# Kernel tuning notes

Measured on AMD Instinct MI355X. Metric: run time of the kernel, lower is better.

Reference implementation:

```python
import jax, jax.numpy as jnp
import numpy as np

SR = 16000
NUM_MEL = 80
FRAME_LEN = 400
FRAME_SHIFT = 160
PADDED_WIN = 512         # next pow2 of 400
NUM_FFT_BINS = PADDED_WIN // 2 + 1  # 257
PREEMPH = 0.97
EPS = 1e-6


def _mel_scale(f):
    return 1127.0 * np.log(1.0 + f / 700.0)


def _get_mel_banks(num_bins, window_padded, sample_freq, low_freq=20.0, high_freq=0.0):
    # Faithful port of torchaudio.compliance.kaldi.get_mel_banks (vtln_warp=1.0)
    num_fft_bins = window_padded // 2  # 256 (last bin padded with zero later)
    nyquist = 0.5 * sample_freq
    if high_freq <= 0.0:
        high_freq = nyquist + high_freq
    fft_bin_width = sample_freq / window_padded
    mel_low = _mel_scale(low_freq)
    mel_high = _mel_scale(high_freq)
    mel_delta = (mel_high - mel_low) / (num_bins + 1)
    left = mel_low + np.arange(num_bins, dtype=np.float64)[:, None] * mel_delta
    center = left + mel_delta
    right = center + mel_delta
    mel = _mel_scale(fft_bin_width * np.arange(num_fft_bins, dtype=np.float64))[None, :]
    up = (mel - left) / (center - left)
    down = (right - mel) / (right - center)
    bins = np.maximum(0.0, np.minimum(up, down))
    return bins.astype(np.float32)  # [num_bins, window_padded//2]


def _make_buffers():
    n = np.arange(FRAME_LEN, dtype=np.float32)
    window = (0.54 - 0.46 * np.cos(2 * np.pi * n / (FRAME_LEN - 1))).astype(np.float32)
    t = np.arange(PADDED_WIN, dtype=np.float32)
    f = np.arange(NUM_FFT_BINS, dtype=np.float32)[:, None]
    angles = 2.0 * np.pi * f * t / PADDED_WIN
    dft_real = np.cos(angles).astype(np.float32)        # [257, 512]
    dft_imag = (-np.sin(angles)).astype(np.float32)     # [257, 512]
    mel = _get_mel_banks(NUM_MEL, PADDED_WIN, float(SR))
    mel_weight = np.pad(mel, ((0, 0), (0, 1)))          # [80, 257]
    return window, dft_real, dft_imag, mel_weight


def setup_inputs() -> dict:
    key = jax.random.key(0)
    waveform = jax.random.normal(key, (32, 480000), dtype=jnp.float32)
    window, dft_real, dft_imag, mel_weight = _make_buffers()
    return {
        "waveform": waveform,
        "window": jnp.asarray(window),
        "dft_real": jnp.asarray(dft_real),
        "dft_imag": jnp.asarray(dft_imag),
        "mel_weight": jnp.asarray(mel_weight),
    }


def reference(waveform, window, dft_real, dft_imag, mel_weight):
    B, T = waveform.shape
    num_frames = (T - FRAME_LEN) // FRAME_SHIFT + 1
    # Framing (equivalent to conv1d with identity kernel, stride=FRAME_SHIFT)
    idx = jnp.arange(num_frames)[:, None] * FRAME_SHIFT + jnp.arange(FRAME_LEN)
    frames = waveform[:, idx].reshape(B * num_frames, FRAME_LEN)  # [BF, 400]
    # dither == 0 -> skipped
    # remove DC offset
    frames = frames - jnp.mean(frames, axis=1, keepdims=True)
    # raw energy (computed by the original module; unused since use_energy=False)
    _log_energy = jnp.log(jnp.maximum(jnp.sum(frames * frames, axis=1), EPS))
    # preemphasis with replicate left pad
    prev = jnp.concatenate([frames[:, :1], frames[:, :-1]], axis=1)
    frames = frames - PREEMPH * prev
    # Hamming window + zero pad to 512
    frames = frames * window[None, :]
    frames = jnp.pad(frames, ((0, 0), (0, PADDED_WIN - FRAME_LEN)))  # [BF, 512]
    # Brute-force DFT as matmuls
    real = frames @ dft_real.T  # [BF, 257]
    imag = frames @ dft_imag.T  # [BF, 257]
    power = real * real + imag * imag
    # Mel projection + log
    mel = power @ mel_weight.T + EPS  # [BF, 80]
    mel = jnp.log(jnp.maximum(mel, EPS))
    return mel.reshape(B, num_frames, NUM_MEL)
```

## Files before the change

kernel.cpp:

```cpp
#include <hip/hip_runtime.h>
#include <math.h>


#define BATCH 32
#define TLEN 480000
#define NFRAMES 2998
#define FL 400
#define FS 160
#define PW 512
#define NM 80
#define MT 32
#define NTILES 94
#define PRE 0.97f
#define EPSF 1e-6f

#define RE_KS 9
#define IM_KS 8
#define RE_U16 (16 * RE_KS * 64 * 8)
#define IM_U16 (16 * IM_KS * 64 * 8)
#define MEL_U16 (6 * 8 * 64 * 8)
#define OFF_REH 0
#define OFF_REL RE_U16
#define OFF_IMH (2 * RE_U16)
#define OFF_IML (2 * RE_U16 + IM_U16)
#define OFF_MEL (2 * RE_U16 + 2 * IM_U16)
#define OFF_CS  (OFF_MEL + MEL_U16)
#define WS_NEED ((size_t)OFF_CS * 2 + 512 * 4)

#define C0_SH 0
#define C0_SL 8704
#define C0_DH 17408
#define C0_DL 26112
#define C1_SH 0
#define C1_SL 10240
#define C1_DH 20480
#define C1_DL 29184

typedef short bf16x8 __attribute__((ext_vector_type(8)));
typedef float f32x4 __attribute__((ext_vector_type(4)));
typedef unsigned int u32;
typedef unsigned short u16;
typedef u32 u32x4 __attribute__((ext_vector_type(4)));

__device__ __forceinline__ u16 f2bf(float f) {
    u32 u = __builtin_bit_cast(u32, f);
    return (u16)((u + 0x7FFFu + ((u >> 16) & 1u)) >> 16);
}
__device__ __forceinline__ float bf2f(u16 h) {
    u32 u = ((u32)h) << 16;
    return __builtin_bit_cast(float, u);
}

__global__ void prep_kernel(const float* __restrict__ dftr, const float* __restrict__ dfti,
                            const float* __restrict__ melw, u16* __restrict__ wsb) {
    int idx = blockIdx.x * 256 + threadIdx.x;
    if (idx < 16 * RE_KS * 64) {
        int nf = idx / (RE_KS * 64);
        int rem = idx - nf * (RE_KS * 64);
        int ks = rem >> 6, l = rem & 63;
        int f = nf * 16 + (l & 15);
        int k = ks * 32 + ((l >> 4) << 3);
        u16* dh = wsb + OFF_REH + (size_t)idx * 8;
        u16* dl = wsb + OFF_REL + (size_t)idx * 8;
        #pragma unroll
        for (int e = 0; e < 8; ++e) {
            int kk = k + e;
            float x = (kk <= 256) ? dftr[(size_t)f * PW + kk] : 0.f;
            u16 h = f2bf(x);
            dh[e] = h;
            dl[e] = f2bf(x - bf2f(h));
        }
    } else if (idx < 16 * RE_KS * 64 + 16 * IM_KS * 64) {
        int j = idx - 16 * RE_KS * 64;
        int nf = j / (IM_KS * 64);
        int rem = j - nf * (IM_KS * 64);
        int ks = rem >> 6, l = rem & 63;
        int f = nf * 16 + (l & 15);
        int k = ks * 32 + ((l >> 4) << 3);
        u16* dh = wsb + OFF_IMH + (size_t)j * 8;
        u16* dl = wsb + OFF_IML + (size_t)j * 8;
        #pragma unroll
        for (int e = 0; e < 8; ++e) {
            float x = dfti[(size_t)f * PW + k + e];
            u16 h = f2bf(x);
            dh[e] = h;
            dl[e] = f2bf(x - bf2f(h));
        }
    } else {
        int m = idx - (16 * RE_KS * 64 + 16 * IM_KS * 64);
        if (m < 6 * 8 * 64) {
            int nf = m / (8 * 64);
            int ks = (m >> 6) & 7, l = m & 63;
            int n = nf * 16 + (l & 15);
            int k = ks * 32 + ((l >> 4) << 3);
            u16* dst = wsb + OFF_MEL + (size_t)m * 8;
            #pragma unroll
            for (int e = 0; e < 8; ++e)
                dst[e] = (n < NM) ? f2bf(melw[(size_t)n * 257 + k + e]) : (u16)0;
        }
    }
}

__global__ void prep_cs_kernel(const float* __restrict__ dftr, const float* __restrict__ dfti,
                               const float* __restrict__ win, u16* __restrict__ wsb) {
    const int gw = (blockIdx.x * 256 + threadIdx.x) >> 6;
    const int lane = threadIdx.x & 63;
    float* cs = (float*)(wsb + OFF_CS);
    float acc = 0.f;
    if (gw < 256) {
        const int f = gw;
        for (int t = lane; t <= 256; t += 64) {
            float wt = (t < FL) ? win[t] : 0.f;
            float wu = (t >= 1 && t < 256 && (512 - t) < FL) ? win[512 - t] : 0.f;
            acc += (wt + wu) * dftr[(size_t)f * PW + t];
        }
    } else {
        const int ff = gw - 256;
        for (int t = lane; t <= 255; t += 64) {
            float wt = (t < FL) ? win[t] : 0.f;
            float wu = (t >= 1 && (512 - t) < FL) ? win[512 - t] : 0.f;
            acc += (wt - wu) * dfti[(size_t)ff * PW + t];
        }
    }
    #pragma unroll
    for (int o = 32; o; o >>= 1) acc += __shfl_xor(acc, o);
    if (lane == 0) cs[gw] = acc;
}

__device__ __forceinline__ u32 swz(int SWT, u32 r) {
    return (SWT == 0) ? ((r & 7u) << 4) : (SWT == 1) ? (((r >> 1) & 3u) << 4) : 0u;
}

#define MFMA6(D, J)                                                                        \
    _Pragma("unroll")                                                                      \
    for (int mf = 0; mf < 2; ++mf) {                                                       \
        acc[mf][J] = __builtin_amdgcn_mfma_f32_16x16x32_bf16(aH[mf], D[0], acc[mf][J], 0, 0, 0); \
        acc[mf][J] = __builtin_amdgcn_mfma_f32_16x16x32_bf16(aL[mf], D[0], acc[mf][J], 0, 0, 0); \
        acc[mf][J] = __builtin_amdgcn_mfma_f32_16x16x32_bf16(aH[mf], D[1], acc[mf][J], 0, 0, 0); \
    }

template<int RS, int SWT, int NKS, int BKS>
__device__ __forceinline__ void dft_pass(
    const char* tH, const char* tL,
    const u16* __restrict__ bH, const u16* __restrict__ bL,
    int ks0, int w, int lane, f32x4 (&acc)[2][2]) {

    bf16x8 aH[2], aL[2], Ba[2], Bb[2];

#define LDA_P(KS)                                                              \
    { _Pragma("unroll")                                                        \
      for (int mf = 0; mf < 2; ++mf) {                                         \
        u32 r = (u32)(mf * 16 + (lane & 15));                                  \
        u32 off = (u32)((KS) * 64 + ((lane >> 4) << 4));                       \
        u32 byte = r * RS + (off ^ swz(SWT, r));                               \
        aH[mf] = *(const bf16x8*)(tH + byte);                                  \
        aL[mf] = *(const bf16x8*)(tL + byte);                                  \
      } }
#define LDB_P(KSG, J, D)                                                       \
    {                                                                          \
        size_t o = ((size_t)((2 * w + (J)) * BKS + (KSG)) * 64 + lane) * 8;    \
        D[0] = *(const bf16x8*)(bH + o);                                       \
        D[1] = *(const bf16x8*)(bL + o);                                       \
    }

    LDB_P(ks0, 0, Ba);
    #pragma unroll
    for (int ks = 0; ks < NKS; ++ks) {
        LDA_P(ks);
        LDB_P(ks0 + ks, 1, Bb);
        MFMA6(Ba, 0);
        if (ks + 1 < NKS) LDB_P(ks0 + ks + 1, 0, Ba);
        MFMA6(Bb, 1);
    }
#undef LDA_P
#undef LDB_P
}

__device__ __forceinline__ void pack_write(const float* ys, char* baseH, char* baseL, u32 byte) {
    u32x4 hv, lv;
    #pragma unroll
    for (int e = 0; e < 4; ++e) {
        u16 h0 = f2bf(ys[2 * e]), h1 = f2bf(ys[2 * e + 1]);
        hv[e] = (u32)h0 | ((u32)h1 << 16);
        u16 l0 = f2bf(ys[2 * e] - bf2f(h0)), l1 = f2bf(ys[2 * e + 1] - bf2f(h1));
        lv[e] = (u32)l0 | ((u32)l1 << 16);
    }
    *(u32x4*)(baseH + byte) = hv;
    *(u32x4*)(baseL + byte) = lv;
}

__global__ __launch_bounds__(512, 4) void fbank_mfma(
    const float* __restrict__ wave, const float* __restrict__ win,
    const u16* __restrict__ wsb, float* __restrict__ out) {
    __shared__ float smean[MT];
    __shared__ u16 stile[18944];
    char* T = (char*)stile;

    const int tid = threadIdx.x, w = tid >> 6, lane = tid & 63;
    const int q = lane >> 4;
    const int cg = lane & 15;
    const int b = blockIdx.y;
    const int f0 = blockIdx.x * MT;
    const float* wb = wave + (size_t)b * TLEN;
    const float4* win4 = (const float4*)win;

    const int rr = w * 4 + q;
    const int fr = f0 + rr;
    const bool valid = fr < NFRAMES;
    const float* x = wb + (size_t)fr * FS;
    const float4* x4 = (const float4*)x;
    float ps = 0.f;

    {
        float4 v0 = {0,0,0,0}, v1 = {0,0,0,0};
        if (valid) { v0 = x4[2 * cg]; v1 = x4[2 * cg + 1]; }
        ps += v0.x + v0.y + v0.z + v0.w + v1.x + v1.y + v1.z + v1.w;
        float4 w0 = win4[2 * cg], w1 = win4[2 * cg + 1];
        float xpn = __shfl(v1.w, lane - 1);
        float xprev = (cg == 0) ? v0.x : xpn;
        float y[8];
        y[0] = (v0.x - PRE * xprev) * w0.x;
        y[1] = (v0.y - PRE * v0.x) * w0.y;
        y[2] = (v0.z - PRE * v0.y) * w0.z;
        y[3] = (v0.w - PRE * v0.z) * w0.w;
        y[4] = (v1.x - PRE * v0.w) * w1.x;
        y[5] = (v1.y - PRE * v1.x) * w1.y;
        y[6] = (v1.z - PRE * v1.y) * w1.z;
        y[7] = (v1.w - PRE * v1.z) * w1.w;

        float yr[8];
        #pragma unroll
        for (int e = 0; e < 8; ++e) yr[e] = 0.f;
        if (cg >= 14) {
            const int u0 = 512 - 8 * cg;
            float4 xr0 = {0,0,0,0}, xr1 = {0,0,0,0};
            float xu0 = 0.f;
            if (valid) {
                xr0 = x4[u0 / 4 - 2]; xr1 = x4[u0 / 4 - 1];
                if (u0 <= 399) xu0 = x[u0];
            }
            ps += xr0.x + xr0.y + xr0.z + xr0.w + xr1.x + xr1.y + xr1.z + xr1.w;
            float4 wr0 = win4[u0 / 4 - 2], wr1 = win4[u0 / 4 - 1];
            float wu0 = (u0 <= 399) ? win[u0] : 0.f;
            yr[0] = (xu0   - PRE * xr1.w) * wu0;
            yr[1] = (xr1.w - PRE * xr1.z) * wr1.w;
            yr[2] = (xr1.z - PRE * xr1.y) * wr1.z;
            yr[3] = (xr1.y - PRE * xr1.x) * wr1.y;
            yr[4] = (xr1.x - PRE * xr0.w) * wr1.x;
            yr[5] = (xr0.w - PRE * xr0.z) * wr0.w;
            yr[6] = (xr0.z - PRE * xr0.y) * wr0.z;
            yr[7] = (xr0.y - PRE * xr0.x) * wr0.y;
        }
        float s8[8], d8[8];
        #pragma unroll
        for (int e = 0; e < 8; ++e) { s8[e] = y[e] + yr[e]; d8[e] = y[e] - yr[e]; }
        u32 byte = (u32)rr * 272u + (u32)cg * 16u;
        pack_write(s8, T + C0_SH, T + C0_SL, byte);
        pack_write(d8, T + C0_DH, T + C0_DL, byte);
    }
    __syncthreads();

    f32x4 accR[2][2], accI[2][2];
    #pragma unroll
    for (int mf = 0; mf < 2; ++mf)
        #pragma unroll
        for (int j = 0; j < 2; ++j) { accR[mf][j] = (f32x4)0.f; accI[mf][j] = (f32x4)0.f; }

    dft_pass<272, 2, 4, RE_KS>(T + C0_SH, T + C0_SL, wsb + OFF_REH, wsb + OFF_REL, 0, w, lane, accR);
    dft_pass<272, 2, 4, IM_KS>(T + C0_DH, T + C0_DL, wsb + OFF_IMH, wsb + OFF_IML, 0, w, lane, accI);
    __syncthreads();

    {
        float4 v0 = {0,0,0,0}, v1 = {0,0,0,0};
        if (valid) { v0 = x4[32 + 2 * cg]; v1 = x4[33 + 2 * cg]; }
        ps += v0.x + v0.y + v0.z + v0.w + v1.x + v1.y + v1.z + v1.w;
        float4 w0 = win4[32 + 2 * cg], w1 = win4[33 + 2 * cg];
        float xpn = __shfl(v1.w, lane - 1);
        float xprev = (cg == 0) ? (valid ? x[127] : 0.f) : xpn;
        float y[8];
        y[0] = (v0.x - PRE * xprev) * w0.x;
        y[1] = (v0.y - PRE * v0.x) * w0.y;
        y[2] = (v0.z - PRE * v0.y) * w0.z;
        y[3] = (v0.w - PRE * v0.z) * w0.w;
        y[4] = (v1.x - PRE * v0.w) * w1.x;
        y[5] = (v1.y - PRE * v1.x) * w1.y;
        y[6] = (v1.z - PRE * v1.y) * w1.z;
        y[7] = (v1.w - PRE * v1.z) * w1.w;

        const int u0 = 384 - 8 * cg;
        float4 xr0 = {0,0,0,0}, xr1 = {0,0,0,0};
        float xu0 = 0.f;
        if (valid) { xr0 = x4[u0 / 4 - 2]; xr1 = x4[u0 / 4 - 1]; xu0 = x[u0]; }
        ps += xr0.x + xr0.y + xr0.z + xr0.w + xr1.x + xr1.y + xr1.z + xr1.w;
        float4 wr0 = win4[u0 / 4 - 2], wr1 = win4[u0 / 4 - 1];
        float wu0 = win[u0];
        float yr[8];
        yr[0] = (xu0   - PRE * xr1.w) * wu0;
        yr[1] = (xr1.w - PRE * xr1.z) * wr1.w;
        yr[2] = (xr1.z - PRE * xr1.y) * wr1.z;
        yr[3] = (xr1.y - PRE * xr1.x) * wr1.y;
        yr[4] = (xr1.x - PRE * xr0.w) * wr1.x;
        yr[5] = (xr0.w - PRE * xr0.z) * wr0.w;
        yr[6] = (xr0.z - PRE * xr0.y) * wr0.z;
        yr[7] = (xr0.y - PRE * xr0.x) * wr0.y;

        float s8[8], d8[8];
        #pragma unroll
        for (int e = 0; e < 8; ++e) { s8[e] = y[e] + yr[e]; d8[e] = y[e] - yr[e]; }
        u32 byteS = (u32)rr * 320u + (((u32)cg * 16u) ^ ((((u32)rr >> 1) & 3u) << 4));
        u32 byteD = (u32)rr * 272u + (u32)cg * 16u;
        pack_write(s8, T + C1_SH, T + C1_SL, byteS);
        pack_write(d8, T + C1_DH, T + C1_DL, byteD);

        float acc = ps;
        #pragma unroll
        for (int o = 8; o; o >>= 1) acc += __shfl_xor(acc, o);
        if (cg == 0) smean[rr] = acc * (1.0f / FL);
    }
    {
        const int trr = tid & 31;
        const int grp = tid >> 5;
        if (grp < 4) {
            const int tfr = f0 + trr;
            float y256 = 0.f;
            if (grp == 0 && tfr < NFRAMES) {
                const float* tx = wb + (size_t)tfr * FS;
                y256 = (tx[256] - PRE * tx[255]) * win[256];
            }
            float s8[8] = {y256, 0.f, 0.f, 0.f, 0.f, 0.f, 0.f, 0.f};
            u32 byte = (u32)trr * 320u + ((((u32)(16 + grp)) * 16u) ^ ((((u32)trr >> 1) & 3u) << 4));
            pack_write(s8, T + C1_SH, T + C1_SL, byte);
        }
    }
    __syncthreads();

    dft_pass<320, 1, 5, RE_KS>(T + C1_SH, T + C1_SL, wsb + OFF_REH, wsb + OFF_REL, 4, w, lane, accR);
    dft_pass<272, 2, 4, IM_KS>(T + C1_DH, T + C1_DL, wsb + OFF_IMH, wsb + OFF_IML, 4, w, lane, accI);
    __syncthreads();

    {
        const float* cs = (const float*)(wsb + OFF_CS);
        #pragma unroll
        for (int mf = 0; mf < 2; ++mf)
            #pragma unroll
            for (int j = 0; j < 2; ++j) {
                const u32 bin = (u32)(32 * w + j * 16 + cg);
                const float Cb = cs[bin], Sb = cs[256 + bin];
                #pragma unroll
                for (int r = 0; r < 4; ++r) {
                    u32 row = (u32)(mf * 16 + (q << 2) + r);
                    const float mcr = (1.0f - PRE) * smean[row];
                    float pR = accR[mf][j][r] - mcr * Cb;
                    float pI = accI[mf][j][r] - mcr * Sb;
                    float pw = pR * pR + pI * pI;
                    u32 byte = (row * 512u + bin * 2u) ^ ((row & 7u) << 4);
                    *(u16*)(T + byte) = f2bf(pw);
                }
            }
    }
    __syncthreads();

    const u16* melb = wsb + OFF_MEL;
    if (w < 6) {
        const int mfm = w & 1;
        const int nf0 = (w >> 1) * 2;
        f32x4 accM[2];
        #pragma unroll
        for (int j = 0; j < 2; ++j) accM[j] = (f32x4)0.f;
        for (int ks = 0; ks < 8; ++ks) {
            u32 row = (u32)(mfm * 16 + cg);
            u32 byte = (row * 512u + (u32)(ks * 32 + (q << 3)) * 2u) ^ ((row & 7u) << 4);
            bf16x8 aP = *(const bf16x8*)(T + byte);
            #pragma unroll
            for (int j = 0; j < 2; ++j) {
                bf16x8 bM = *(const bf16x8*)(melb + ((size_t)((nf0 + j) * 8 + ks) * 64 + lane) * 8);
                accM[j] = __builtin_amdgcn_mfma_f32_16x16x32_bf16(aP, bM, accM[j], 0, 0, 0);
            }
        }
        #pragma unroll
        for (int j = 0; j < 2; ++j) {
            const int m = (nf0 + j) * 16 + cg;
            #pragma unroll
            for (int r = 0; r < 4; ++r) {
                const int rowl = mfm * 16 + (q << 2) + r;
                const int ofr = f0 + rowl;
                if (ofr < NFRAMES && m < NM) {
                    float v = fmaxf(accM[j][r] + EPSF, EPSF);
                    out[((size_t)b * NFRAMES + ofr) * NM + m] = logf(v);
                }
            }
        }
    }
}

#define TFB 16
#define NB 256
__global__ __launch_bounds__(256, 3) void fbank_fallback(
    const float* __restrict__ wave, const float* __restrict__ win,
    const float* __restrict__ dftr, const float* __restrict__ dfti,
    const float* __restrict__ melw, float* __restrict__ out) {
    __shared__ float s_fr[TFB][PW];
    __shared__ float s_pw[TFB][NB + 1];
    const int tid = threadIdx.x, wv = tid >> 6, lane = tid & 63;
    const int fbase = blockIdx.x * TFB;
    #pragma unroll
    for (int j = 0; j < TFB / 4; ++j) {
        const int lf = wv * (TFB / 4) + j;
        const int gid = fbase + lf;
        const int bb = gid / NFRAMES;
        const int fr = gid - bb * NFRAMES;
        const float* x = wave + (size_t)bb * TLEN + (size_t)fr * FS;
        float s = 0.f;
        for (int i = lane; i < FL; i += 64) s += x[i];
        #pragma unroll
        for (int off = 32; off >= 1; off >>= 1) s += __shfl_xor(s, off);
        const float mean = s * (1.0f / FL);
        for (int i = lane; i < FL; i += 64) {
            const float xi = x[i];
            const float xm = (i == 0) ? xi : x[i - 1];
            s_fr[lf][i] = (xi - PRE * xm - (1.0f - PRE) * mean) * win[i];
        }
        for (int i = FL + lane; i < PW; i += 64) s_fr[lf][i] = 0.f;
    }
    __syncthreads();
    {
        const int bin = tid;
        const float4* dr4 = (const float4*)(dftr + (size_t)bin * PW);
        const float4* di4 = (const float4*)(dfti + (size_t)bin * PW);
        float accr[TFB], acci[TFB];
        #pragma unroll
        for (int f = 0; f < TFB; ++f) { accr[f] = 0.f; acci[f] = 0.f; }
        for (int k4 = 0; k4 < PW / 4; ++k4) {
            const float4 r = dr4[k4], im = di4[k4];
            #pragma unroll
            for (int f = 0; f < TFB; ++f) {
                const float4 fr = *(const float4*)&s_fr[f][k4 * 4];
                accr[f] += fr.x * r.x + fr.y * r.y + fr.z * r.z + fr.w * r.w;
                acci[f] += fr.x * im.x + fr.y * im.y + fr.z * im.z + fr.w * im.w;
            }
        }
        #pragma unroll
        for (int f = 0; f < TFB; ++f) s_pw[f][bin] = accr[f] * accr[f] + acci[f] * acci[f];
    }
    __syncthreads();
    for (int o = tid; o < TFB * NM; o += 256) {
        const int f = o / NM, m = o - f * NM;
        const float* wm = melw + (size_t)m * 257;
        float acc = 0.f;
        for (int k = 0; k < NB; ++k) acc += s_pw[f][k] * wm[k];
        out[(size_t)(fbase + f) * NM + m] = logf(fmaxf(acc + EPSF, EPSF));
    }
}

extern "C" void kernel_launch(void* const* d_in, const int* in_sizes, int n_in,
                              void* d_out, int out_size, void* d_ws, size_t ws_size,
                              hipStream_t stream) {
    const float* wave = (const float*)d_in[0];
    const float* win  = (const float*)d_in[1];
    const float* dftr = (const float*)d_in[2];
    const float* dfti = (const float*)d_in[3];
    const float* melw = (const float*)d_in[4];
    float* out = (float*)d_out;

    if (ws_size >= WS_NEED) {
        u16* wsb = (u16*)d_ws;
        const int prep_threads = 16 * RE_KS * 64 + 16 * IM_KS * 64 + 6 * 8 * 64;
        prep_kernel<<<(prep_threads + 255) / 256, 256, 0, stream>>>(dftr, dfti, melw, wsb);
        prep_cs_kernel<<<128, 256, 0, stream>>>(dftr, dfti, win, wsb);
        dim3 grid(NTILES, BATCH);
        fbank_mfma<<<grid, 512, 0, stream>>>(wave, win, wsb, out);
    } else {
        const int nblocks = (BATCH * NFRAMES) / TFB;
        fbank_fallback<<<nblocks, 256, 0, stream>>>(wave, win, dftr, dfti, melw, out);
    }
}
```

Baseline: 119.1 us.

## Enlarge frame tile to 48 rows and use hardware bf16 pack conversion

Raises the per-block frame tile from 32 to 48 rows, so each wave runs three M-fragments per DFT pass. Each bf16 B-fragment loaded from global memory is then reused across more MFMAs, and there are fewer blocks overall. The packing and mel stages are restructured so the first four waves handle the extra 16 rows. The software float-to-bf16 rounding is replaced by the v_cvt_pk_bf16_f32 instruction. In exchange, LDS use and register pressure grow, which may lower occupancy under the 512x4 launch bounds, and waves 4-7 sit idle during the extra packing.

```diff
diff --git a/kernel.cpp b/kernel.cpp
--- a/kernel.cpp
+++ b/kernel.cpp
@@ -9,8 +9,8 @@
 #define FS 160
 #define PW 512
 #define NM 80
-#define MT 32
-#define NTILES 94
+#define MT 48
+#define NTILES 63
 #define PRE 0.97f
 #define EPSF 1e-6f
 
@@ -28,13 +28,13 @@
 #define WS_NEED ((size_t)OFF_CS * 2 + 512 * 4)
 
 #define C0_SH 0
-#define C0_SL 8704
-#define C0_DH 17408
-#define C0_DL 26112
+#define C0_SL 13056
+#define C0_DH 26112
+#define C0_DL 39168
 #define C1_SH 0
-#define C1_SL 10240
-#define C1_DH 20480
-#define C1_DL 29184
+#define C1_SL 15360
+#define C1_DH 30720
+#define C1_DL 43776
 
 typedef short bf16x8 __attribute__((ext_vector_type(8)));
 typedef float f32x4 __attribute__((ext_vector_type(4)));
@@ -49,6 +49,11 @@
 __device__ __forceinline__ float bf2f(u16 h) {
     u32 u = ((u32)h) << 16;
     return __builtin_bit_cast(float, u);
+}
+__device__ __forceinline__ u32 cvtpk2(float lo, float hi) {
+    u32 r;
+    asm("v_cvt_pk_bf16_f32 %0, %1, %2" : "=v"(r) : "v"(lo), "v"(hi));
+    return r;
 }
 
 __global__ void prep_kernel(const float* __restrict__ dftr, const float* __restrict__ dfti,
@@ -131,25 +136,25 @@
     return (SWT == 0) ? ((r & 7u) << 4) : (SWT == 1) ? (((r >> 1) & 3u) << 4) : 0u;
 }
 
-#define MFMA6(D, J)                                                                        \
+#define MFMA9(D, J)                                                                        \
     _Pragma("unroll")                                                                      \
-    for (int mf = 0; mf < 2; ++mf) {                                                       \
+    for (int mf = 0; mf < 3; ++mf) {                                                       \
         acc[mf][J] = __builtin_amdgcn_mfma_f32_16x16x32_bf16(aH[mf], D[0], acc[mf][J], 0, 0, 0); \
         acc[mf][J] = __builtin_amdgcn_mfma_f32_16x16x32_bf16(aL[mf], D[0], acc[mf][J], 0, 0, 0); \
         acc[mf][J] = __builtin_amdgcn_mfma_f32_16x16x32_bf16(aH[mf], D[1], acc[mf][J], 0, 0, 0); \
     }
 
 template<int RS, int SWT, int NKS, int BKS>
-__device__ __forceinline__ void dft_pass(
+__device__ __forceinline__ void dft_pass3(
     const char* tH, const char* tL,
     const u16* __restrict__ bH, const u16* __restrict__ bL,
-    int ks0, int w, int lane, f32x4 (&acc)[2][2]) {
-
-    bf16x8 aH[2], aL[2], Ba[2], Bb[2];
+    int ks0, int w, int lane, f32x4 (&acc)[3][2]) {
+
+    bf16x8 aH[3], aL[3], Ba[2], Bb[2];
 
 #define LDA_P(KS)                                                              \
     { _Pragma("unroll")                                                        \
-      for (int mf = 0; mf < 2; ++mf) {                                         \
+      for (int mf = 0; mf < 3; ++mf) {                                         \
         u32 r = (u32)(mf * 16 + (lane & 15));                                  \
         u32 off = (u32)((KS) * 64 + ((lane >> 4) << 4));                       \
         u32 byte = r * RS + (off ^ swz(SWT, r));                               \
@@ -168,9 +173,9 @@
     for (int ks = 0; ks < NKS; ++ks) {
         LDA_P(ks);
         LDB_P(ks0 + ks, 1, Bb);
-        MFMA6(Ba, 0);
+        MFMA9(Ba, 0);
         if (ks + 1 < NKS) LDB_P(ks0 + ks + 1, 0, Ba);
-        MFMA6(Bb, 1);
+        MFMA9(Bb, 1);
     }
 #undef LDA_P
 #undef LDB_P
@@ -180,121 +185,56 @@
     u32x4 hv, lv;
     #pragma unroll
     for (int e = 0; e < 4; ++e) {
-        u16 h0 = f2bf(ys[2 * e]), h1 = f2bf(ys[2 * e + 1]);
-        hv[e] = (u32)h0 | ((u32)h1 << 16);
-        u16 l0 = f2bf(ys[2 * e] - bf2f(h0)), l1 = f2bf(ys[2 * e + 1] - bf2f(h1));
-        lv[e] = (u32)l0 | ((u32)l1 << 16);
+        float y0 = ys[2 * e], y1 = ys[2 * e + 1];
+        u32 h = cvtpk2(y0, y1);
+        hv[e] = h;
+        float h0 = __builtin_bit_cast(float, h << 16);
+        float h1 = __builtin_bit_cast(float, h & 0xFFFF0000u);
+        lv[e] = cvtpk2(y0 - h0, y1 - h1);
     }
     *(u32x4*)(baseH + byte) = hv;
     *(u32x4*)(baseL + byte) = lv;
 }
 
-__global__ __launch_bounds__(512, 4) void fbank_mfma(
-    const float* __restrict__ wave, const float* __restrict__ win,
-    const u16* __restrict__ wsb, float* __restrict__ out) {
-    __shared__ float smean[MT];
-    __shared__ u16 stile[18944];
-    char* T = (char*)stile;
-
-    const int tid = threadIdx.x, w = tid >> 6, lane = tid & 63;
-    const int q = lane >> 4;
-    const int cg = lane & 15;
-    const int b = blockIdx.y;
-    const int f0 = blockIdx.x * MT;
-    const float* wb = wave + (size_t)b * TLEN;
-    const float4* win4 = (const float4*)win;
-
-    const int rr = w * 4 + q;
+__device__ __forceinline__ float pack_c0(const float* wb, const float4* win4,
+                                         const float* win, char* T,
+                                         int f0, int rr, int lane, int cg) {
     const int fr = f0 + rr;
     const bool valid = fr < NFRAMES;
     const float* x = wb + (size_t)fr * FS;
     const float4* x4 = (const float4*)x;
     float ps = 0.f;
 
-    {
-        float4 v0 = {0,0,0,0}, v1 = {0,0,0,0};
-        if (valid) { v0 = x4[2 * cg]; v1 = x4[2 * cg + 1]; }
-        ps += v0.x + v0.y + v0.z + v0.w + v1.x + v1.y + v1.z + v1.w;
-        float4 w0 = win4[2 * cg], w1 = win4[2 * cg + 1];
-        float xpn = __shfl(v1.w, lane - 1);
-        float xprev = (cg == 0) ? v0.x : xpn;
-        float y[8];
-        y[0] = (v0.x - PRE * xprev) * w0.x;
-        y[1] = (v0.y - PRE * v0.x) * w0.y;
-        y[2] = (v0.z - PRE * v0.y) * w0.z;
-        y[3] = (v0.w - PRE * v0.z) * w0.w;
-        y[4] = (v1.x - PRE * v0.w) * w1.x;
-        y[5] = (v1.y - PRE * v1.x) * w1.y;
-        y[6] = (v1.z - PRE * v1.y) * w1.z;
-        y[7] = (v1.w - PRE * v1.z) * w1.w;
-
-        float yr[8];
-        #pragma unroll
-        for (int e = 0; e < 8; ++e) yr[e] = 0.f;
-        if (cg >= 14) {
-            const int u0 = 512 - 8 * cg;
-            float4 xr0 = {0,0,0,0}, xr1 = {0,0,0,0};
-            float xu0 = 0.f;
-            if (valid) {
-                xr0 = x4[u0 / 4 - 2]; xr1 = x4[u0 / 4 - 1];
-                if (u0 <= 399) xu0 = x[u0];
-            }
-            ps += xr0.x + xr0.y + xr0.z + xr0.w + xr1.x + xr1.y + xr1.z + xr1.w;
-            float4 wr0 = win4[u0 / 4 - 2], wr1 = win4[u0 / 4 - 1];
-            float wu0 = (u0 <= 399) ? win[u0] : 0.f;
-            yr[0] = (xu0   - PRE * xr1.w) * wu0;
-            yr[1] = (xr1.w - PRE * xr1.z) * wr1.w;
-            yr[2] = (xr1.z - PRE * xr1.y) * wr1.z;
-            yr[3] = (xr1.y - PRE * xr1.x) * wr1.y;
-            yr[4] = (xr1.x - PRE * xr0.w) * wr1.x;
-            yr[5] = (xr0.w - PRE * xr0.z) * wr0.w;
-            yr[6] = (xr0.z - PRE * xr0.y) * wr0.z;
-            yr[7] = (xr0.y - PRE * xr0.x) * wr0.y;
-        }
-        float s8[8], d8[8];
-        #pragma unroll
-        for (int e = 0; e < 8; ++e) { s8[e] = y[e] + yr[e]; d8[e] = y[e] - yr[e]; }
-        u32 byte = (u32)rr * 272u + (u32)cg * 16u;
-        pack_write(s8, T + C0_SH, T + C0_SL, byte);
-        pack_write(d8, T + C0_DH, T + C0_DL, byte);
-    }
-    __syncthreads();
-
-    f32x4 accR[2][2], accI[2][2];
-    #pragma unroll
-    for (int mf = 0; mf < 2; ++mf)
-        #pragma unroll
-        for (int j = 0; j < 2; ++j) { accR[mf][j] = (f32x4)0.f; accI[mf][j] = (f32x4)0.f; }
-
-    dft_pass<272, 2, 4, RE_KS>(T + C0_SH, T + C0_SL, wsb + OFF_REH, wsb + OFF_REL, 0, w, lane, accR);
-    dft_pass<272, 2, 4, IM_KS>(T + C0_DH, T + C0_DL, wsb + OFF_IMH, wsb + OFF_IML, 0, w, lane, accI);
-    __syncthreads();
-
-    {
-        float4 v0 = {0,0,0,0}, v1 = {0,0,0,0};
-        if (valid) { v0 = x4[32 + 2 * cg]; v1 = x4[33 + 2 * cg]; }
-        ps += v0.x + v0.y + v0.z + v0.w + v1.x + v1.y + v1.z + v1.w;
-        float4 w0 = win4[32 + 2 * cg], w1 = win4[33 + 2 * cg];
-        float xpn = __shfl(v1.w, lane - 1);
-        float xprev = (cg == 0) ? (valid ? x[127] : 0.f) : xpn;
-        float y[8];
-        y[0] = (v0.x - PRE * xprev) * w0.x;
-        y[1] = (v0.y - PRE * v0.x) * w0.y;
-        y[2] = (v0.z - PRE * v0.y) * w0.z;
-        y[3] = (v0.w - PRE * v0.z) * w0.w;
-        y[4] = (v1.x - PRE * v0.w) * w1.x;
-        y[5] = (v1.y - PRE * v1.x) * w1.y;
-        y[6] = (v1.z - PRE * v1.y) * w1.z;
-        y[7] = (v1.w - PRE * v1.z) * w1.w;
-
-        const int u0 = 384 - 8 * cg;
+    float4 v0 = {0,0,0,0}, v1 = {0,0,0,0};
+    if (valid) { v0 = x4[2 * cg]; v1 = x4[2 * cg + 1]; }
+    ps += v0.x + v0.y + v0.z + v0.w + v1.x + v1.y + v1.z + v1.w;
+    float4 w0 = win4[2 * cg], w1 = win4[2 * cg + 1];
+    float xpn = __shfl(v1.w, lane - 1);
+    float xprev = (cg == 0) ? v0.x : xpn;
+    float y[8];
+    y[0] = (v0.x - PRE * xprev) * w0.x;
+    y[1] = (v0.y - PRE * v0.x) * w0.y;
+    y[2] = (v0.z - PRE * v0.y) * w0.z;
+    y[3] = (v0.w - PRE * v0.z) * w0.w;
+    y[4] = (v1.x - PRE * v0.w) * w1.x;
+    y[5] = (v1.y - PRE * v1.x) * w1.y;
+    y[6] = (v1.z - PRE * v1.y) * w1.z;
+    y[7] = (v1.w - PRE * v1.z) * w1.w;
+
+    float yr[8];
+    #pragma unroll
+    for (int e = 0; e < 8; ++e) yr[e] = 0.f;
+    if (cg >= 14) {
+        const int u0 = 512 - 8 * cg;
         float4 xr0 = {0,0,0,0}, xr1 = {0,0,0,0};
         float xu0 = 0.f;
-        if (valid) { xr0 = x4[u0 / 4 - 2]; xr1 = x4[u0 / 4 - 1]; xu0 = x[u0]; }
+        if (valid) {
+            xr0 = x4[u0 / 4 - 2]; xr1 = x4[u0 / 4 - 1];
+            if (u0 <= 399) xu0 = x[u0];
+        }
         ps += xr0.x + xr0.y + xr0.z + xr0.w + xr1.x + xr1.y + xr1.z + xr1.w;
         float4 wr0 = win4[u0 / 4 - 2], wr1 = win4[u0 / 4 - 1];
-        float wu0 = win[u0];
-        float yr[8];
+        float wu0 = (u0 <= 399) ? win[u0] : 0.f;
         yr[0] = (xu0   - PRE * xr1.w) * wu0;
         yr[1] = (xr1.w - PRE * xr1.z) * wr1.w;
         yr[2] = (xr1.z - PRE * xr1.y) * wr1.z;
@@ -303,45 +243,137 @@
         yr[5] = (xr0.w - PRE * xr0.z) * wr0.w;
         yr[6] = (xr0.z - PRE * xr0.y) * wr0.z;
         yr[7] = (xr0.y - PRE * xr0.x) * wr0.y;
-
-        float s8[8], d8[8];
-        #pragma unroll
-        for (int e = 0; e < 8; ++e) { s8[e] = y[e] + yr[e]; d8[e] = y[e] - yr[e]; }
-        u32 byteS = (u32)rr * 320u + (((u32)cg * 16u) ^ ((((u32)rr >> 1) & 3u) << 4));
-        u32 byteD = (u32)rr * 272u + (u32)cg * 16u;
-        pack_write(s8, T + C1_SH, T + C1_SL, byteS);
-        pack_write(d8, T + C1_DH, T + C1_DL, byteD);
-
-        float acc = ps;
-        #pragma unroll
-        for (int o = 8; o; o >>= 1) acc += __shfl_xor(acc, o);
-        if (cg == 0) smean[rr] = acc * (1.0f / FL);
-    }
+    }
+    float s8[8], d8[8];
+    #pragma unroll
+    for (int e = 0; e < 8; ++e) { s8[e] = y[e] + yr[e]; d8[e] = y[e] - yr[e]; }
+    u32 byte = (u32)rr * 272u + (u32)cg * 16u;
+    pack_write(s8, T + C0_SH, T + C0_SL, byte);
+    pack_write(d8, T + C0_DH, T + C0_DL, byte);
+    return ps;
+}
+
+__device__ __forceinline__ float pack_c1(const float* wb, const float4* win4,
+                                         const float* win, char* T,
+                                         int f0, int rr, int lane, int cg) {
+    const int fr = f0 + rr;
+    const bool valid = fr < NFRAMES;
+    const float* x = wb + (size_t)fr * FS;
+    const float4* x4 = (const float4*)x;
+    float ps = 0.f;
+
+    float4 v0 = {0,0,0,0}, v1 = {0,0,0,0};
+    if (valid) { v0 = x4[32 + 2 * cg]; v1 = x4[33 + 2 * cg]; }
+    ps += v0.x + v0.y + v0.z + v0.w + v1.x + v1.y + v1.z + v1.w;
+    float4 w0 = win4[32 + 2 * cg], w1 = win4[33 + 2 * cg];
+    float xpn = __shfl(v1.w, lane - 1);
+    float xprev = (cg == 0) ? (valid ? x[127] : 0.f) : xpn;
+    float y[8];
+    y[0] = (v0.x - PRE * xprev) * w0.x;
+    y[1] = (v0.y - PRE * v0.x) * w0.y;
+    y[2] = (v0.z - PRE * v0.y) * w0.z;
+    y[3] = (v0.w - PRE * v0.z) * w0.w;
+    y[4] = (v1.x - PRE * v0.w) * w1.x;
+    y[5] = (v1.y - PRE * v1.x) * w1.y;
+    y[6] = (v1.z - PRE * v1.y) * w1.z;
+    y[7] = (v1.w - PRE * v1.z) * w1.w;
+
+    const int u0 = 384 - 8 * cg;
+    float4 xr0 = {0,0,0,0}, xr1 = {0,0,0,0};
+    float xu0 = 0.f;
+    if (valid) { xr0 = x4[u0 / 4 - 2]; xr1 = x4[u0 / 4 - 1]; xu0 = x[u0]; }
+    ps += xr0.x + xr0.y + xr0.z + xr0.w + xr1.x + xr1.y + xr1.z + xr1.w;
+    float4 wr0 = win4[u0 / 4 - 2], wr1 = win4[u0 / 4 - 1];
+    float wu0 = win[u0];
+    float yr[8];
+    yr[0] = (xu0   - PRE * xr1.w) * wu0;
+    yr[1] = (xr1.w - PRE * xr1.z) * wr1.w;
+    yr[2] = (xr1.z - PRE * xr1.y) * wr1.z;
+    yr[3] = (xr1.y - PRE * xr1.x) * wr1.y;
+    yr[4] = (xr1.x - PRE * xr0.w) * wr1.x;
+    yr[5] = (xr0.w - PRE * xr0.z) * wr0.w;
+    yr[6] = (xr0.z - PRE * xr0.y) * wr0.z;
+    yr[7] = (xr0.y - PRE * xr0.x) * wr0.y;
+
+    float s8[8], d8[8];
+    #pragma unroll
+    for (int e = 0; e < 8; ++e) { s8[e] = y[e] + yr[e]; d8[e] = y[e] - yr[e]; }
+    u32 byteS = (u32)rr * 320u + (((u32)cg * 16u) ^ ((((u32)rr >> 1) & 3u) << 4));
+    u32 byteD = (u32)rr * 272u + (u32)cg * 16u;
+    pack_write(s8, T + C1_SH, T + C1_SL, byteS);
+    pack_write(d8, T + C1_DH, T + C1_DL, byteD);
+    return ps;
+}
+
+__global__ __launch_bounds__(512, 4) void fbank_mfma(
+    const float* __restrict__ wave, const float* __restrict__ win,
+    const u16* __restrict__ wsb, float* __restrict__ out) {
+    __shared__ float smean[MT];
+    __shared__ u16 stile[28416];
+    char* T = (char*)stile;
+
+    const int tid = threadIdx.x, w = tid >> 6, lane = tid & 63;
+    const int q = lane >> 4;
+    const int cg = lane & 15;
+    const int b = blockIdx.y;
+    const int f0 = blockIdx.x * MT;
+    const float* wb = wave + (size_t)b * TLEN;
+    const float4* win4 = (const float4*)win;
+
+    const int rrA = w * 4 + q;
+    const int rrB = 32 + rrA;
+
+    float psA = pack_c0(wb, win4, win, T, f0, rrA, lane, cg);
+    float psB = 0.f;
+    if (w < 4) psB = pack_c0(wb, win4, win, T, f0, rrB, lane, cg);
+    __syncthreads();
+
+    f32x4 accR[3][2], accI[3][2];
+    #pragma unroll
+    for (int mf = 0; mf < 3; ++mf)
+        #pragma unroll
+        for (int j = 0; j < 2; ++j) { accR[mf][j] = (f32x4)0.f; accI[mf][j] = (f32x4)0.f; }
+
+    dft_pass3<272, 2, 4, RE_KS>(T + C0_SH, T + C0_SL, wsb + OFF_REH, wsb + OFF_REL, 0, w, lane, accR);
+    dft_pass3<272, 2, 4, IM_KS>(T + C0_DH, T + C0_DL, wsb + OFF_IMH, wsb + OFF_IML, 0, w, lane, accI);
+    __syncthreads();
+
+    psA += pack_c1(wb, win4, win, T, f0, rrA, lane, cg);
+    if (w < 4) psB += pack_c1(wb, win4, win, T, f0, rrB, lane, cg);
     {
-        const int trr = tid & 31;
-        const int grp = tid >> 5;
-        if (grp < 4) {
-            const int tfr = f0 + trr;
-            float y256 = 0.f;
-            if (grp == 0 && tfr < NFRAMES) {
-                const float* tx = wb + (size_t)tfr * FS;
-                y256 = (tx[256] - PRE * tx[255]) * win[256];
-            }
-            float s8[8] = {y256, 0.f, 0.f, 0.f, 0.f, 0.f, 0.f, 0.f};
-            u32 byte = (u32)trr * 320u + ((((u32)(16 + grp)) * 16u) ^ ((((u32)trr >> 1) & 3u) << 4));
-            pack_write(s8, T + C1_SH, T + C1_SL, byte);
-        }
-    }
-    __syncthreads();
-
-    dft_pass<320, 1, 5, RE_KS>(T + C1_SH, T + C1_SL, wsb + OFF_REH, wsb + OFF_REL, 4, w, lane, accR);
-    dft_pass<272, 2, 4, IM_KS>(T + C1_DH, T + C1_DL, wsb + OFF_IMH, wsb + OFF_IML, 4, w, lane, accI);
+        float a = psA;
+        #pragma unroll
+        for (int o = 8; o; o >>= 1) a += __shfl_xor(a, o);
+        if (cg == 0) smean[rrA] = a * (1.0f / FL);
+    }
+    if (w < 4) {
+        float a = psB;
+        #pragma unroll
+        for (int o = 8; o; o >>= 1) a += __shfl_xor(a, o);
+        if (cg == 0) smean[rrB] = a * (1.0f / FL);
+    }
+    if (w < 4 && lane < MT) {
+        const int trr = lane;
+        const int tfr = f0 + trr;
+        float y256 = 0.f;
+        if (w == 0 && tfr < NFRAMES) {
+            const float* tx = wb + (size_t)tfr * FS;
+            y256 = (tx[256] - PRE * tx[255]) * win[256];
+        }
+        float s8[8] = {y256, 0.f, 0.f, 0.f, 0.f, 0.f, 0.f, 0.f};
+        u32 byte = (u32)trr * 320u + ((((u32)(16 + w)) * 16u) ^ ((((u32)trr >> 1) & 3u) << 4));
+        pack_write(s8, T + C1_SH, T + C1_SL, byte);
+    }
+    __syncthreads();
+
+    dft_pass3<320, 1, 5, RE_KS>(T + C1_SH, T + C1_SL, wsb + OFF_REH, wsb + OFF_REL, 4, w, lane, accR);
+    dft_pass3<272, 2, 4, IM_KS>(T + C1_DH, T + C1_DL, wsb + OFF_IMH, wsb + OFF_IML, 4, w, lane, accI);
     __syncthreads();
 
     {
         const float* cs = (const float*)(wsb + OFF_CS);
         #pragma unroll
-        for (int mf = 0; mf < 2; ++mf)
+        for (int mf = 0; mf < 3; ++mf)
             #pragma unroll
             for (int j = 0; j < 2; ++j) {
                 const u32 bin = (u32)(32 * w + j * 16 + cg);
@@ -362,23 +394,23 @@
 
     const u16* melb = wsb + OFF_MEL;
     if (w < 6) {
-        const int mfm = w & 1;
-        const int nf0 = (w >> 1) * 2;
-        f32x4 accM[2];
-        #pragma unroll
-        for (int j = 0; j < 2; ++j) accM[j] = (f32x4)0.f;
+        const int mfm = w >> 1;
+        const int nf0 = (w & 1) * 3;
+        f32x4 accM[3];
+        #pragma unroll
+        for (int j = 0; j < 3; ++j) accM[j] = (f32x4)0.f;
         for (int ks = 0; ks < 8; ++ks) {
             u32 row = (u32)(mfm * 16 + cg);
             u32 byte = (row * 512u + (u32)(ks * 32 + (q << 3)) * 2u) ^ ((row & 7u) << 4);
             bf16x8 aP = *(const bf16x8*)(T + byte);
             #pragma unroll
-            for (int j = 0; j < 2; ++j) {
+            for (int j = 0; j < 3; ++j) {
                 bf16x8 bM = *(const bf16x8*)(melb + ((size_t)((nf0 + j) * 8 + ks) * 64 + lane) * 8);
                 accM[j] = __builtin_amdgcn_mfma_f32_16x16x32_bf16(aP, bM, accM[j], 0, 0, 0);
             }
         }
         #pragma unroll
-        for (int j = 0; j < 2; ++j) {
+        for (int j = 0; j < 3; ++j) {
             const int m = (nf0 + j) * 16 + cg;
             #pragma unroll
             for (int r = 0; r < 4; ++r) {
```

New measurement: 113.8 us. 4.5% less time.
